# Kernel optimization log

Hardware: AMD Instinct MI355X
Metric: run time of the kernel (lower is better)

Reference implementation:

```python
import jax, jax.numpy as jnp
import numpy as np

L, H, D, M = 2, 8, 64, 64   # layers, heads, query dim, value dim
DM = H * M                  # d_model = 512
FF = 1024                   # feed-forward dim
B, S, F_IN = 8, 4096, 586   # batch, seq_len, input feature dim
EPS_ATTN = 1e-6             # fast_transformers LinearAttention eps
EPS_LN = 1e-5               # torch LayerNorm default eps


def setup_inputs() -> dict:
    key = jax.random.key(0)
    ks = jax.random.split(key, 16)
    p = lambda k, shape: jax.random.normal(k, shape, jnp.float32) * 0.02
    return {
        "embeddings": jax.random.normal(ks[0], (B, S, F_IN), jnp.float32),
        "W0": p(ks[1], (F_IN, DM)), "b0": jnp.zeros((DM,), jnp.float32),
        "Wq": p(ks[2], (L, DM, DM)), "bq": jnp.zeros((L, DM), jnp.float32),
        "Wk": p(ks[3], (L, DM, DM)), "bk": jnp.zeros((L, DM), jnp.float32),
        "Wv": p(ks[4], (L, DM, DM)), "bv": jnp.zeros((L, DM), jnp.float32),
        "Wo": p(ks[5], (L, DM, DM)), "bo": jnp.zeros((L, DM), jnp.float32),
        "ln1_s": jnp.ones((L, DM), jnp.float32), "ln1_b": jnp.zeros((L, DM), jnp.float32),
        "W1": p(ks[6], (L, DM, FF)), "b1": jnp.zeros((L, FF), jnp.float32),
        "W2": p(ks[7], (L, FF, DM)), "b2": jnp.zeros((L, DM), jnp.float32),
        "ln2_s": jnp.ones((L, DM), jnp.float32), "ln2_b": jnp.zeros((L, DM), jnp.float32),
        "lnf_s": jnp.ones((DM,), jnp.float32), "lnf_b": jnp.zeros((DM,), jnp.float32),
        "Wout": p(ks[8], (DM, 1)), "bout": jnp.zeros((1,), jnp.float32),
    }


def _ln(x, s, b):
    mu = x.mean(-1, keepdims=True)
    var = ((x - mu) ** 2).mean(-1, keepdims=True)
    return (x - mu) * jax.lax.rsqrt(var + EPS_LN) * s + b


def _feat(x):
    # elu feature map of fast_transformers linear attention
    return jax.nn.elu(x) + 1.0


def reference(embeddings, W0, b0, Wq, bq, Wk, bk, Wv, bv, Wo, bo,
              ln1_s, ln1_b, W1, b1, W2, b2, ln2_s, ln2_b,
              lnf_s, lnf_b, Wout, bout):
    x = embeddings @ W0 + b0                       # [B,S,DM]
    Bn, Sn = x.shape[0], x.shape[1]
    for l in range(L):
        q = _feat((x @ Wq[l] + bq[l]).reshape(Bn, Sn, H, D))
        k = _feat((x @ Wk[l] + bk[l]).reshape(Bn, Sn, H, D))
        v = (x @ Wv[l] + bv[l]).reshape(Bn, Sn, H, M)
        # non-causal linear attention: O(S) in sequence length
        kv = jnp.einsum("bshd,bshm->bhdm", k, v)                    # [B,H,D,M]
        z = 1.0 / (jnp.einsum("blhd,bhd->blh", q, k.sum(1)) + EPS_ATTN)
        a = jnp.einsum("blhd,bhdm,blh->blhm", q, kv, z).reshape(Bn, Sn, DM)
        x = x + a @ Wo[l] + bo[l]                  # residual (dropout=0 eval)
        x = _ln(x, ln1_s[l], ln1_b[l])
        y = jax.nn.relu(x @ W1[l] + b1[l]) @ W2[l] + b2[l]
        x = _ln(x + y, ln2_s[l], ln2_b[l])
    x = _ln(x, lnf_s, lnf_b)                        # final encoder LayerNorm
    return (x @ Wout + bout)[..., 0]                # squeeze -> [B,S]
```

## Files before the change

### kernel.cpp

```cpp
#include <hip/hip_runtime.h>
#include <hip/hip_bf16.h>
#include <math.h>

typedef unsigned short u16;
typedef short s16x8 __attribute__((ext_vector_type(8)));
typedef float f32x4 __attribute__((ext_vector_type(4)));

#define BS_   32768
#define SEQ_  4096
#define DM_   512
#define FF_   1024
#define FIN_  586
#define FINP_ 640
#define PADC  136
#define PADB  520
#define NCH   8

__device__ __forceinline__ u16 f2b(float f) {
    __hip_bfloat16 h = __float2bfloat16(f);
    return *reinterpret_cast<u16*>(&h);
}
__device__ __forceinline__ float b2f(u16 h) {
    union { unsigned u; float f; } a; a.u = ((unsigned)h) << 16;
    return a.f;
}

typedef __attribute__((address_space(1))) const unsigned gu32;
typedef __attribute__((address_space(3))) unsigned lu32;
__device__ __forceinline__ void glds16(const void* g, void* l) {
    __builtin_amdgcn_global_load_lds((gu32*)g, (lu32*)l, 16, 0, 0);
}

__device__ __forceinline__ void tr_tile(const float* __restrict__ W, u16* __restrict__ Wt,
                                        int K, int N, int Kpad, int tidx, int ktiles,
                                        float (*t)[33]) {
    int kb = (tidx % ktiles) << 5, nb = (tidx / ktiles) << 5;
    int tx = threadIdx.x, ty = threadIdx.y;
#pragma unroll
    for (int j = 0; j < 32; j += 8) {
        int k = kb + ty + j;
        t[ty + j][tx] = (k < K) ? W[(size_t)k * N + nb + tx] : 0.f;
    }
    __syncthreads();
#pragma unroll
    for (int j = 0; j < 32; j += 8) {
        Wt[(size_t)(nb + ty + j) * Kpad + kb + tx] = f2b(t[tx][ty + j]);
    }
}

__global__ void k_tr_all(const float* __restrict__ W0, const float* __restrict__ Wq,
                         const float* __restrict__ Wk, const float* __restrict__ Wv,
                         const float* __restrict__ Wo, const float* __restrict__ W1,
                         const float* __restrict__ W2,
                         u16* __restrict__ W0t, u16* __restrict__ Wqkv,
                         u16* __restrict__ Wot, u16* __restrict__ W1t,
                         u16* __restrict__ W2t) {
    __shared__ float t[32][33];
    int b = blockIdx.x;
    if (b < 320) { tr_tile(W0, W0t, FIN_, DM_, FINP_, b, 20, t); return; }
    b -= 320;
    int l = b >> 11;
    int r = b & 2047;
    if (r < 768) {
        int sel = r >> 8, ti = r & 255;
        const float* src = sel == 0 ? Wq : (sel == 1 ? Wk : Wv);
        tr_tile(src + (size_t)l * 262144, Wqkv + (size_t)l * 786432 + (size_t)sel * 262144,
                512, 512, 512, ti, 16, t);
    } else if (r < 1024) {
        tr_tile(Wo + (size_t)l * 262144, Wot + (size_t)l * 262144, 512, 512, 512, r - 768, 16, t);
    } else if (r < 1536) {
        tr_tile(W1 + (size_t)l * 524288, W1t + (size_t)l * 524288, 512, 1024, 512, r - 1024, 16, t);
    } else {
        tr_tile(W2 + (size_t)l * 524288, W2t + (size_t)l * 524288, 1024, 512, 1024, r - 1536, 32, t);
    }
}

__global__ __launch_bounds__(256)
void k_emb(const float* __restrict__ E, u16* __restrict__ Ep) {
    const int total8 = BS_ * (FINP_ / 8);
    for (int i = blockIdx.x * 256 + threadIdx.x; i < total8; i += gridDim.x * 256) {
        int rr = i / (FINP_ / 8), c = (i % (FINP_ / 8)) * 8;
        const float* rp = E + (size_t)rr * FIN_ + c;
        s16x8 o;
#pragma unroll
        for (int e = 0; e < 8; ++e) {
            float v = (c + e < FIN_) ? rp[e] : 0.f;
            o[e] = (short)f2b(v);
        }
        *(s16x8*)(Ep + (size_t)rr * FINP_ + c) = o;
    }
}

template<int EPI>
__global__ __launch_bounds__(256, 4)
void k_gemm(const u16* __restrict__ A, const u16* __restrict__ Bt,
            const float* __restrict__ bias0, const float* __restrict__ bias1,
            const float* __restrict__ bias2,
            u16* __restrict__ out0, u16* __restrict__ out1, u16* __restrict__ out2,
            int M, int N, int K, int NT) {
    __shared__ __align__(16) u16 smem[16384];
    u16* sC = smem;

    const int nwg = gridDim.x;
    const int cpx = nwg >> 3;
    const int wg = (blockIdx.x & 7) * cpx + (blockIdx.x >> 3);
    const int mt = wg / NT, nt = wg - mt * NT;
    const int m0 = mt << 7, n0 = nt << 7;
    const int tid = threadIdx.x;
    const int w = tid >> 6, l = tid & 63;
    const int wm = (w >> 1) << 6, wn = (w & 1) << 6;
    const int lr = l & 15, lg = l >> 4;

    const int srow = tid >> 2;
    const int swz = (((tid & 3) ^ ((srow >> 1) & 3)) & 3) << 3;
    const u16* Ap = A + (size_t)(m0 + srow) * K + swz;
    const u16* Bp = Bt + (size_t)(n0 + srow) * K + swz;

    auto stage = [&](int d, int tt) {
        const size_t ko = (size_t)tt << 5;
        u16* da = smem + d * 4096 + tid * 8;
        u16* db = smem + 8192 + d * 4096 + tid * 8;
        glds16(Ap + ko, da);
        glds16(Ap + ko + (size_t)64 * K, da + 2048);
        glds16(Bp + ko, db);
        glds16(Bp + ko + (size_t)64 * K, db + 2048);
    };

    const int axk = ((lg ^ ((lr >> 1) & 3)) & 3) << 3;

    f32x4 acc[4][4] = {};
    const int ntile = K >> 5;

    stage(0, 0);
    __syncthreads();

    for (int t = 0; t < ntile; ++t) {
        const int d = t & 1;
        if (t + 1 < ntile) stage(d ^ 1, t + 1);
        const u16* sA = smem + d * 4096;
        const u16* sB = smem + 8192 + d * 4096;
        s16x8 af[4], bfr[4];
#pragma unroll
        for (int i = 0; i < 4; ++i) af[i] = *(const s16x8*)(sA + (wm + i * 16 + lr) * 32 + axk);
#pragma unroll
        for (int j = 0; j < 4; ++j) bfr[j] = *(const s16x8*)(sB + (wn + j * 16 + lr) * 32 + axk);
        __builtin_amdgcn_s_setprio(1);
#pragma unroll
        for (int i = 0; i < 4; ++i)
#pragma unroll
            for (int j = 0; j < 4; ++j)
                acc[i][j] = __builtin_amdgcn_mfma_f32_16x16x32_bf16(af[i], bfr[j], acc[i][j], 0, 0, 0);
        __builtin_amdgcn_s_setprio(0);
        __syncthreads();
    }

    const int seg = (EPI == 1) ? (n0 >> 9) : 0;
    const float* bias = (EPI == 1) ? (seg == 0 ? bias0 : (seg == 1 ? bias1 : bias2)) : bias0;
    u16* dst = (EPI == 1) ? (seg == 0 ? out0 : (seg == 1 ? out1 : out2)) : out0;
    const int ldo = (EPI == 1) ? 512 : N;
    const int ncol0 = (EPI == 1) ? (n0 & 511) : n0;

#pragma unroll
    for (int pass = 0; pass < 2; ++pass) {
        if ((w >> 1) == pass) {
#pragma unroll
            for (int j = 0; j < 4; ++j) {
                const int col = wn + j * 16 + lr;
                const float bv = bias[ncol0 + col];
#pragma unroll
                for (int i = 0; i < 4; ++i)
#pragma unroll
                    for (int r = 0; r < 4; ++r) {
                        const int row = i * 16 + (lg << 2) + r;
                        sC[row * PADC + col] = f2b(acc[i][j][r] + bv);
                    }
            }
        }
        __syncthreads();
        const int rbase = m0 + (pass << 6);
#pragma unroll
        for (int t = 0; t < 4; ++t) {
            const int idx = t * 256 + tid;
            const int row = idx >> 4;
            const int c8 = (idx & 15) << 3;
            s16x8 v8 = *(const s16x8*)(sC + row * PADC + c8);
            size_t gaddr = (size_t)(rbase + row) * ldo + ncol0 + c8;
            s16x8 o = v8;
            if constexpr (EPI == 1) {
                if (seg < 2) {
#pragma unroll
                    for (int e = 0; e < 8; ++e) {
                        float v = b2f((u16)v8[e]);
                        v = (v > 0.f) ? v + 1.f : __expf(v);
                        o[e] = (short)f2b(v);
                    }
                }
            } else if constexpr (EPI == 3) {
#pragma unroll
                for (int e = 0; e < 8; ++e)
                    o[e] = (short)f2b(fmaxf(b2f((u16)v8[e]), 0.f));
            }
            *(s16x8*)(dst + gaddr) = o;
        }
        __syncthreads();
    }
}

template<int K>
__global__ __launch_bounds__(512, 4)
void k_gemm_ln(const u16* __restrict__ A, const u16* __restrict__ Bt,
               const float* __restrict__ bias, const u16* __restrict__ resid,
               const float* __restrict__ g, const float* __restrict__ be,
               u16* __restrict__ xb) {
    __shared__ __align__(16) u16 smem[36864];
    u16* sC = smem;

    const int nwg = gridDim.x;
    const int cpx = nwg >> 3;
    const int wg = (blockIdx.x & 7) * cpx + (blockIdx.x >> 3);
    const int m0 = wg << 6;
    const int tid = threadIdx.x;
    const int w = tid >> 6, l = tid & 63;
    const int wn = w << 6;
    const int lr = l & 15, lg = l >> 4;

    const int srow = tid >> 2;
    const int swz = (((tid & 3) ^ ((srow >> 1) & 3)) & 3) << 3;
    const u16* ApA = A + (size_t)(m0 + (srow & 63)) * K + ((((tid & 3) ^ (((srow & 63) >> 1) & 3)) & 3) << 3);
    const u16* BpB = Bt + (size_t)srow * K + swz;

    auto stage = [&](int d, int tt) {
        const size_t ko = (size_t)tt << 5;
        if (tid < 256) glds16(ApA + ko, smem + d * 2048 + tid * 8);
#pragma unroll
        for (int c = 0; c < 4; ++c)
            glds16(BpB + ko + (size_t)(c * 128) * K,
                   smem + 4096 + d * 16384 + c * 4096 + tid * 8);
    };

    const int axk = ((lg ^ ((lr >> 1) & 3)) & 3) << 3;

    f32x4 acc[4][4] = {};
    const int ntile = K >> 5;

    stage(0, 0);
    __syncthreads();

    for (int t = 0; t < ntile; ++t) {
        const int d = t & 1;
        if (t + 1 < ntile) stage(d ^ 1, t + 1);
        const u16* sA = smem + d * 2048;
        const u16* sB = smem + 4096 + d * 16384 + wn * 32;
        s16x8 af[4], bfr[4];
#pragma unroll
        for (int i = 0; i < 4; ++i) af[i] = *(const s16x8*)(sA + (i * 16 + lr) * 32 + axk);
#pragma unroll
        for (int j = 0; j < 4; ++j) bfr[j] = *(const s16x8*)(sB + (j * 16 + lr) * 32 + axk);
        __builtin_amdgcn_s_setprio(1);
#pragma unroll
        for (int i = 0; i < 4; ++i)
#pragma unroll
            for (int j = 0; j < 4; ++j)
                acc[i][j] = __builtin_amdgcn_mfma_f32_16x16x32_bf16(af[i], bfr[j], acc[i][j], 0, 0, 0);
        __builtin_amdgcn_s_setprio(0);
        __syncthreads();
    }

#pragma unroll
    for (int j = 0; j < 4; ++j) {
        const int col = wn + j * 16 + lr;
        const float bv = bias[col];
#pragma unroll
        for (int i = 0; i < 4; ++i)
#pragma unroll
            for (int r = 0; r < 4; ++r) {
                const int row = i * 16 + (lg << 2) + r;
                sC[row * PADB + col] = f2b(acc[i][j][r] + bv);
            }
    }
    __syncthreads();

#pragma unroll
    for (int it = 0; it < 8; ++it) {
        const int row = it * 8 + w;
        s16x8 cv = *(const s16x8*)(sC + row * PADB + l * 8);
        s16x8 rv = *(const s16x8*)(resid + (size_t)(m0 + row) * DM_ + l * 8);
        float x[8];
#pragma unroll
        for (int e = 0; e < 8; ++e) x[e] = b2f((u16)cv[e]) + b2f((u16)rv[e]);
        float sum = 0.f;
#pragma unroll
        for (int e = 0; e < 8; ++e) sum += x[e];
#pragma unroll
        for (int off = 32; off > 0; off >>= 1) sum += __shfl_xor(sum, off);
        float mu = sum * (1.f / DM_);
        float sq = 0.f;
#pragma unroll
        for (int e = 0; e < 8; ++e) { float d = x[e] - mu; sq += d * d; }
#pragma unroll
        for (int off = 32; off > 0; off >>= 1) sq += __shfl_xor(sq, off);
        float rs = rsqrtf(sq * (1.f / DM_) + 1e-5f);
        const int c = l * 8;
        const f32x4* gp = (const f32x4*)(g + c);
        const f32x4* bp = (const f32x4*)(be + c);
        f32x4 g0 = gp[0], g1 = gp[1], e0 = bp[0], e1 = bp[1];
        s16x8 pk;
#pragma unroll
        for (int e = 0; e < 4; ++e) pk[e] = (short)f2b((x[e] - mu) * rs * g0[e] + e0[e]);
#pragma unroll
        for (int e = 0; e < 4; ++e) pk[4 + e] = (short)f2b((x[4 + e] - mu) * rs * g1[e] + e1[e]);
        *(s16x8*)(xb + (size_t)(m0 + row) * DM_ + c) = pk;
    }
}

__global__ __launch_bounds__(256)
void k_kv(const u16* __restrict__ kb_, const u16* __restrict__ vb_,
          float* __restrict__ kvp, float* __restrict__ ksump) {
    __shared__ float sk[64 * 68], sv[64 * 68];
    int bh = blockIdx.x, b = bh >> 3, h = bh & 7;
    int ch = blockIdx.y;
    int tid = threadIdx.x;
    int d0 = (tid & 15) << 2, m0 = (tid >> 4) << 2;
    float acc[4][4] = {};
    float ks[4] = {0.f, 0.f, 0.f, 0.f};
    size_t gbase = ((size_t)b * SEQ_ + (size_t)ch * (SEQ_ / NCH)) * DM_ + h * 64;

    for (int st = 0; st < SEQ_ / NCH; st += 64) {
#pragma unroll
        for (int i = 0; i < 2; ++i) {
            int li = tid + (i << 8);
            int r = li >> 3, c8 = (li & 7) << 3;
            s16x8 kv_ = *(const s16x8*)(kb_ + gbase + (size_t)(st + r) * DM_ + c8);
            s16x8 vv_ = *(const s16x8*)(vb_ + gbase + (size_t)(st + r) * DM_ + c8);
#pragma unroll
            for (int e = 0; e < 8; ++e) {
                sk[r * 68 + c8 + e] = b2f((u16)kv_[e]);
                sv[r * 68 + c8 + e] = b2f((u16)vv_[e]);
            }
        }
        __syncthreads();
        for (int s = 0; s < 64; ++s) {
            f32x4 kd = *(const f32x4*)(sk + s * 68 + d0);
            f32x4 vm = *(const f32x4*)(sv + s * 68 + m0);
#pragma unroll
            for (int i = 0; i < 4; ++i)
#pragma unroll
                for (int j = 0; j < 4; ++j) acc[i][j] += kd[i] * vm[j];
            if ((tid >> 4) == 0) { ks[0] += kd[0]; ks[1] += kd[1]; ks[2] += kd[2]; ks[3] += kd[3]; }
        }
        __syncthreads();
    }
    float* kvo = kvp + ((size_t)ch * 64 + bh) * 4096;
#pragma unroll
    for (int i = 0; i < 4; ++i)
#pragma unroll
        for (int j = 0; j < 4; ++j) kvo[(d0 + i) * 64 + m0 + j] = acc[i][j];
    if ((tid >> 4) == 0) {
        float* kso = ksump + ((size_t)ch * 64 + bh) * 64;
#pragma unroll
        for (int e = 0; e < 4; ++e) kso[d0 + e] = ks[e];
    }
}

__global__ __launch_bounds__(256)
void k_attn(const u16* __restrict__ qb_, const float* __restrict__ kvp,
            const float* __restrict__ ksump, u16* __restrict__ ab_) {
    __shared__ float skv[64 * 64];
    __shared__ float sq[64 * 65];
    __shared__ float sks[64];
    int tid = threadIdx.x;
    int bh = blockIdx.y, b = bh >> 3, h = bh & 7;
    int s0 = blockIdx.x << 6;

    for (int i = tid; i < 4096; i += 256) {
        float v = 0.f;
#pragma unroll
        for (int c = 0; c < NCH; ++c) v += kvp[((size_t)c * 64 + bh) * 4096 + i];
        skv[i] = v;
    }
    if (tid < 64) {
        float v = 0.f;
#pragma unroll
        for (int c = 0; c < NCH; ++c) v += ksump[((size_t)c * 64 + bh) * 64 + tid];
        sks[tid] = v;
    }
#pragma unroll
    for (int i = 0; i < 2; ++i) {
        int li = tid + (i << 8);
        int r = li >> 3, c8 = (li & 7) << 3;
        s16x8 v = *(const s16x8*)(qb_ + ((size_t)b * SEQ_ + s0 + r) * DM_ + h * 64 + c8);
#pragma unroll
        for (int e = 0; e < 8; ++e) sq[r * 65 + c8 + e] = b2f((u16)v[e]);
    }
    __syncthreads();

    int sl = tid >> 2, m0 = (tid & 3) << 4;
    float den = 0.f;
    for (int d = 0; d < 64; ++d) den += sq[sl * 65 + d] * sks[d];
    float z = 1.f / (den + 1e-6f);

    float acc[16] = {};
    for (int d = 0; d < 64; ++d) {
        float qv = sq[sl * 65 + d];
        const f32x4* kp = (const f32x4*)(skv + d * 64 + m0);
#pragma unroll
        for (int j4 = 0; j4 < 4; ++j4) {
            f32x4 kv4 = kp[j4];
#pragma unroll
            for (int e = 0; e < 4; ++e) acc[j4 * 4 + e] += qv * kv4[e];
        }
    }
    u16* op = ab_ + ((size_t)b * SEQ_ + s0 + sl) * DM_ + h * 64 + m0;
    s16x8 o0, o1;
#pragma unroll
    for (int e = 0; e < 8; ++e) o0[e] = (short)f2b(acc[e] * z);
#pragma unroll
    for (int e = 0; e < 8; ++e) o1[e] = (short)f2b(acc[8 + e] * z);
    *(s16x8*)op = o0;
    *(s16x8*)(op + 8) = o1;
}

__global__ __launch_bounds__(256)
void k_final(const u16* __restrict__ in, const float* __restrict__ gf,
             const float* __restrict__ bf_, const float* __restrict__ wout,
             const float* __restrict__ bout, float* __restrict__ out) {
    int row = blockIdx.x * 4 + (threadIdx.x >> 6);
    int l = threadIdx.x & 63;
    s16x8 raw = *(const s16x8*)(in + (size_t)row * DM_ + l * 8);
    float x[8];
#pragma unroll
    for (int e = 0; e < 8; ++e) x[e] = b2f((u16)raw[e]);
    float sum = 0.f;
#pragma unroll
    for (int e = 0; e < 8; ++e) sum += x[e];
#pragma unroll
    for (int off = 32; off > 0; off >>= 1) sum += __shfl_xor(sum, off);
    float mu = sum * (1.f / DM_);
    float sq = 0.f;
#pragma unroll
    for (int e = 0; e < 8; ++e) { float d = x[e] - mu; sq += d * d; }
#pragma unroll
    for (int off = 32; off > 0; off >>= 1) sq += __shfl_xor(sq, off);
    float rs = rsqrtf(sq * (1.f / DM_) + 1e-5f);
    int c = l * 8;
    float p = 0.f;
#pragma unroll
    for (int e = 0; e < 8; ++e)
        p += ((x[e] - mu) * rs * gf[c + e] + bf_[c + e]) * wout[c + e];
#pragma unroll
    for (int off = 32; off > 0; off >>= 1) p += __shfl_xor(p, off);
    if (l == 0) out[row] = p + bout[0];
}

extern "C" void kernel_launch(void* const* d_in, const int* in_sizes, int n_in,
                              void* d_out, int out_size, void* d_ws, size_t ws_size,
                              hipStream_t stream) {
    const float* emb   = (const float*)d_in[0];
    const float* W0    = (const float*)d_in[1];
    const float* b0    = (const float*)d_in[2];
    const float* Wq    = (const float*)d_in[3];
    const float* bq    = (const float*)d_in[4];
    const float* Wk    = (const float*)d_in[5];
    const float* bk    = (const float*)d_in[6];
    const float* Wv    = (const float*)d_in[7];
    const float* bv    = (const float*)d_in[8];
    const float* Wo    = (const float*)d_in[9];
    const float* bo    = (const float*)d_in[10];
    const float* ln1s  = (const float*)d_in[11];
    const float* ln1b  = (const float*)d_in[12];
    const float* W1    = (const float*)d_in[13];
    const float* b1    = (const float*)d_in[14];
    const float* W2    = (const float*)d_in[15];
    const float* b2    = (const float*)d_in[16];
    const float* ln2s  = (const float*)d_in[17];
    const float* ln2b  = (const float*)d_in[18];
    const float* lnfs  = (const float*)d_in[19];
    const float* lnfb  = (const float*)d_in[20];
    const float* Wout  = (const float*)d_in[21];
    const float* bout  = (const float*)d_in[22];
    float* out = (float*)d_out;

    char* ws = (char*)d_ws;
    size_t off = 0;
    auto alloc = [&](size_t bytes) -> void* {
        void* p = ws + off;
        off += (bytes + 255) & ~(size_t)255;
        return p;
    };
    u16* xb   = (u16*)alloc((size_t)BS_ * DM_ * 2);
    u16* qb   = (u16*)alloc((size_t)BS_ * DM_ * 2);
    u16* kb   = (u16*)alloc((size_t)BS_ * DM_ * 2);
    u16* vb   = (u16*)alloc((size_t)BS_ * DM_ * 2);
    float* kvp   = (float*)alloc((size_t)NCH * 64 * 4096 * 4);
    float* ksump = (float*)alloc((size_t)NCH * 64 * 64 * 4);
    u16* wp   = (u16*)alloc((size_t)4521984 * 2);

    u16* ab   = vb;
    u16* h1b  = kb;
    u16* embp = kb;

    u16* W0t  = wp;
    u16* Wqkv = wp + 327680;
    u16* Wot  = Wqkv + 2 * 786432;
    u16* W1t  = Wot + 2 * 262144;
    u16* W2t  = W1t + 2 * 524288;

    k_tr_all<<<4416, dim3(32, 8), 0, stream>>>(W0, Wq, Wk, Wv, Wo, W1, W2,
                                               W0t, Wqkv, Wot, W1t, W2t);
    k_emb<<<2560, 256, 0, stream>>>(emb, embp);

    k_gemm<0><<<1024, 256, 0, stream>>>(embp, W0t, b0, nullptr, nullptr,
                                        xb, nullptr, nullptr, BS_, DM_, FINP_, 4);

    for (int l = 0; l < 2; ++l) {
        k_gemm<1><<<3072, 256, 0, stream>>>(xb, Wqkv + (size_t)l * 786432,
                                            bq + l * 512, bk + l * 512, bv + l * 512,
                                            qb, kb, vb, BS_, 1536, 512, 12);
        k_kv<<<dim3(64, NCH), 256, 0, stream>>>(kb, vb, kvp, ksump);
        k_attn<<<dim3(64, 64), 256, 0, stream>>>(qb, kvp, ksump, ab);
        k_gemm_ln<512><<<512, 512, 0, stream>>>(ab, Wot + (size_t)l * 262144,
                                                bo + l * 512, xb,
                                                ln1s + l * 512, ln1b + l * 512, xb);
        k_gemm<3><<<2048, 256, 0, stream>>>(xb, W1t + (size_t)l * 524288,
                                            b1 + l * 1024, nullptr, nullptr,
                                            h1b, nullptr, nullptr, BS_, 1024, 512, 8);
        k_gemm_ln<1024><<<512, 512, 0, stream>>>(h1b, W2t + (size_t)l * 524288,
                                                 b2 + l * 512, xb,
                                                 ln2s + l * 512, ln2b + l * 512, xb);
    }
    k_final<<<8192, 256, 0, stream>>>(xb, lnfs, lnfb, Wout, bout, out);
}
```

Before: 701.5 us.

## Split KV chunk reduction into own kernel and use bf16 MFMA for attention apply

The per-chunk KV partial sums are now reduced once per batch-head in a separate kernel that writes a transposed, XOR-swizzled bf16 KV matrix and a summed key vector. Previously every attention block re-reduced all chunks. The attention kernel now handles 256 rows per block, loads Q and KV into swizzled LDS with direct global-to-LDS copies, and computes Q·KV with 16x16x32 bf16 MFMA instead of scalar FP32 FMAs. Output is staged through LDS for coalesced stores. This adds a kernel launch and rounds KV to bf16, which costs some precision.

```diff
diff --git a/kernel.cpp b/kernel.cpp
--- a/kernel.cpp
+++ b/kernel.cpp
@@ -363,61 +363,108 @@
 }
 
 __global__ __launch_bounds__(256)
-void k_attn(const u16* __restrict__ qb_, const float* __restrict__ kvp,
-            const float* __restrict__ ksump, u16* __restrict__ ab_) {
-    __shared__ float skv[64 * 64];
-    __shared__ float sq[64 * 65];
+void k_red(const float* __restrict__ kvp, const float* __restrict__ ksump,
+           u16* __restrict__ kvt, float* __restrict__ ksum) {
+    int bh = blockIdx.x, q = blockIdx.y;
+    int tid = threadIdx.x;
+#pragma unroll
+    for (int p = 0; p < 4; ++p) {
+        int i = (q * 4 + p) * 256 + tid;
+        float v = 0.f;
+#pragma unroll
+        for (int c = 0; c < NCH; ++c) v += kvp[((size_t)c * 64 + bh) * 4096 + i];
+        int d = i >> 6, m = i & 63;
+        int slot = ((d >> 3) ^ (m & 7)) & 7;
+        kvt[(size_t)bh * 4096 + m * 64 + slot * 8 + (d & 7)] = f2b(v);
+    }
+    if (q == 0 && tid < 64) {
+        float v = 0.f;
+#pragma unroll
+        for (int c = 0; c < NCH; ++c) v += ksump[((size_t)c * 64 + bh) * 64 + tid];
+        ksum[bh * 64 + tid] = v;
+    }
+}
+
+__global__ __launch_bounds__(256)
+void k_attn(const u16* __restrict__ qb_, const u16* __restrict__ kvt,
+            const float* __restrict__ ksum, u16* __restrict__ ab_) {
+    __shared__ __align__(16) u16 qs[256 * 64];
+    __shared__ __align__(16) u16 skv[64 * 64];
+    __shared__ float sden[256];
     __shared__ float sks[64];
-    int tid = threadIdx.x;
-    int bh = blockIdx.y, b = bh >> 3, h = bh & 7;
-    int s0 = blockIdx.x << 6;
-
-    for (int i = tid; i < 4096; i += 256) {
-        float v = 0.f;
-#pragma unroll
-        for (int c = 0; c < NCH; ++c) v += kvp[((size_t)c * 64 + bh) * 4096 + i];
-        skv[i] = v;
-    }
-    if (tid < 64) {
-        float v = 0.f;
-#pragma unroll
-        for (int c = 0; c < NCH; ++c) v += ksump[((size_t)c * 64 + bh) * 64 + tid];
-        sks[tid] = v;
-    }
-#pragma unroll
-    for (int i = 0; i < 2; ++i) {
-        int li = tid + (i << 8);
-        int r = li >> 3, c8 = (li & 7) << 3;
-        s16x8 v = *(const s16x8*)(qb_ + ((size_t)b * SEQ_ + s0 + r) * DM_ + h * 64 + c8);
-#pragma unroll
-        for (int e = 0; e < 8; ++e) sq[r * 65 + c8 + e] = b2f((u16)v[e]);
-    }
-    __syncthreads();
-
-    int sl = tid >> 2, m0 = (tid & 3) << 4;
-    float den = 0.f;
-    for (int d = 0; d < 64; ++d) den += sq[sl * 65 + d] * sks[d];
-    float z = 1.f / (den + 1e-6f);
-
-    float acc[16] = {};
-    for (int d = 0; d < 64; ++d) {
-        float qv = sq[sl * 65 + d];
-        const f32x4* kp = (const f32x4*)(skv + d * 64 + m0);
-#pragma unroll
-        for (int j4 = 0; j4 < 4; ++j4) {
-            f32x4 kv4 = kp[j4];
-#pragma unroll
-            for (int e = 0; e < 4; ++e) acc[j4 * 4 + e] += qv * kv4[e];
-        }
-    }
-    u16* op = ab_ + ((size_t)b * SEQ_ + s0 + sl) * DM_ + h * 64 + m0;
-    s16x8 o0, o1;
-#pragma unroll
-    for (int e = 0; e < 8; ++e) o0[e] = (short)f2b(acc[e] * z);
-#pragma unroll
-    for (int e = 0; e < 8; ++e) o1[e] = (short)f2b(acc[8 + e] * z);
-    *(s16x8*)op = o0;
-    *(s16x8*)(op + 8) = o1;
+    const int tid = threadIdx.x;
+    const int bh = blockIdx.y, b = bh >> 3, h = bh & 7;
+    const int s0 = blockIdx.x << 8;
+    const int w = tid >> 6, l = tid & 63;
+    const int lr = l & 15, lg = l >> 4;
+
+    {
+        const int srw = tid >> 3, ch = tid & 7;
+        const int scol = ((ch ^ (srw & 7)) & 7) << 3;
+        const u16* qsrc = qb_ + ((size_t)b * SEQ_ + s0 + srw) * DM_ + h * 64 + scol;
+#pragma unroll
+        for (int p = 0; p < 8; ++p)
+            glds16(qsrc + (size_t)(p * 32) * DM_, qs + p * 2048 + tid * 8);
+#pragma unroll
+        for (int p = 0; p < 2; ++p)
+            glds16(kvt + (size_t)bh * 4096 + p * 2048 + tid * 8, skv + p * 2048 + tid * 8);
+    }
+    if (tid < 64) sks[tid] = ksum[bh * 64 + tid];
+    __syncthreads();
+
+    {
+        const int row = (w << 6) + l;
+        float den = 0.f;
+#pragma unroll
+        for (int c = 0; c < 8; ++c) {
+            s16x8 qv = *(const s16x8*)(qs + row * 64 + (((c ^ (row & 7)) & 7) << 3));
+#pragma unroll
+            for (int e = 0; e < 8; ++e) den += b2f((u16)qv[e]) * sks[c * 8 + e];
+        }
+        sden[row] = 1.f / (den + 1e-6f);
+    }
+    __syncthreads();
+
+    f32x4 acc[4][4] = {};
+#pragma unroll
+    for (int kh = 0; kh < 2; ++kh) {
+        const int c = kh * 4 + lg;
+        s16x8 bfr[4];
+#pragma unroll
+        for (int j = 0; j < 4; ++j) {
+            const int mm = j * 16 + lr;
+            bfr[j] = *(const s16x8*)(skv + mm * 64 + (((c ^ (mm & 7)) & 7) << 3));
+        }
+#pragma unroll
+        for (int i = 0; i < 4; ++i) {
+            const int rr = (w << 6) + i * 16 + lr;
+            s16x8 af = *(const s16x8*)(qs + rr * 64 + (((c ^ (rr & 7)) & 7) << 3));
+#pragma unroll
+            for (int j = 0; j < 4; ++j)
+                acc[i][j] = __builtin_amdgcn_mfma_f32_16x16x32_bf16(af, bfr[j], acc[i][j], 0, 0, 0);
+        }
+    }
+    __syncthreads();
+
+#pragma unroll
+    for (int i = 0; i < 4; ++i) {
+#pragma unroll
+        for (int r = 0; r < 4; ++r) {
+            const int row = (w << 6) + i * 16 + (lg << 2) + r;
+            const float z = sden[row];
+#pragma unroll
+            for (int j = 0; j < 4; ++j)
+                qs[row * 64 + j * 16 + lr] = f2b(acc[i][j][r] * z);
+        }
+    }
+    __syncthreads();
+    {
+        const int srw = tid >> 3, ch = tid & 7;
+        u16* odst = ab_ + ((size_t)b * SEQ_ + s0 + srw) * DM_ + h * 64 + ch * 8;
+#pragma unroll
+        for (int p = 0; p < 8; ++p)
+            *(s16x8*)(odst + (size_t)(p * 32) * DM_) = *(const s16x8*)(qs + p * 2048 + tid * 8);
+    }
 }
 
 __global__ __launch_bounds__(256)
@@ -493,6 +540,8 @@
     u16* vb   = (u16*)alloc((size_t)BS_ * DM_ * 2);
     float* kvp   = (float*)alloc((size_t)NCH * 64 * 4096 * 4);
     float* ksump = (float*)alloc((size_t)NCH * 64 * 64 * 4);
+    u16* kvt  = (u16*)alloc((size_t)64 * 4096 * 2);
+    float* ksum = (float*)alloc((size_t)64 * 64 * 4);
     u16* wp   = (u16*)alloc((size_t)4521984 * 2);
 
     u16* ab   = vb;
@@ -517,7 +566,8 @@
                                             bq + l * 512, bk + l * 512, bv + l * 512,
                                             qb, kb, vb, BS_, 1536, 512, 12);
         k_kv<<<dim3(64, NCH), 256, 0, stream>>>(kb, vb, kvp, ksump);
-        k_attn<<<dim3(64, 64), 256, 0, stream>>>(qb, kvp, ksump, ab);
+        k_red<<<dim3(64, 4), 256, 0, stream>>>(kvp, ksump, kvt, ksum);
+        k_attn<<<dim3(16, 64), 256, 0, stream>>>(qb, kvt, ksum, ab);
         k_gemm_ln<512><<<512, 512, 0, stream>>>(ab, Wot + (size_t)l * 262144,
                                                 bo + l * 512, xb,
                                                 ln1s + l * 512, ln1b + l * 512, xb);
```

Result: faster. 601.7 us (-14.2%).
